# Kernel optimization log

Hardware: AMD Instinct MI355X
Metric: run time of the kernel (lower is better)

The kernel has to match this reference:

```python
import jax, jax.numpy as jnp
import numpy as np

N_PTS = 65534      # 2**16 - 2 from rand_subset
N_VARS = 24        # len(mesh.full_varlist); cols 0/1/2 = lat_deg/lon_deg/reltime_hours
RES = 1.0          # config.latent_res (degrees)
GH, GW = 180, 360  # len(latent_lats), len(latent_lons)
CL = 512           # config.latent_size
TR_DIM, TR_TOK, DEPTH, HEADS, DH = 128, 4, 2, 8, 16
PE_NUM = 8         # DEFAULT_POSEMB_NUM
DA_HALF = 12.0     # mesh.da_window_size / 2
EMB_IN = N_VARS + 3 * (1 + 2 * PE_NUM)  # 75


def setup_inputs() -> dict:
    key = jax.random.key(0)
    ks = jax.random.split(key, 12)
    feats = jax.random.normal(ks[0], (N_PTS, N_VARS), dtype=jnp.float32) * 0.5
    lat = jax.random.uniform(ks[1], (N_PTS,), minval=-90.0, maxval=90.0)
    lon = jax.random.uniform(ks[2], (N_PTS,), minval=-180.0, maxval=180.0)
    t = jax.random.uniform(ks[3], (N_PTS,), minval=-12.0, maxval=12.0)
    x = feats.at[:, 0].set(lat).at[:, 1].set(lon).at[:, 2].set(t)
    w = lambda k, s: jax.random.normal(k, s, dtype=jnp.float32) * 0.02
    return dict(
        x=x,
        W_emb=w(ks[4], (EMB_IN, TR_DIM * TR_TOK)), b_emb=jnp.zeros(TR_DIM * TR_TOK),
        ln1_s=jnp.ones((DEPTH, TR_DIM)), ln1_b=jnp.zeros((DEPTH, TR_DIM)),
        Wqkv=w(ks[5], (DEPTH, TR_DIM, 3 * TR_DIM)), bqkv=jnp.zeros((DEPTH, 3 * TR_DIM)),
        Wo=w(ks[6], (DEPTH, TR_DIM, TR_DIM)), bo=jnp.zeros((DEPTH, TR_DIM)),
        ln2_s=jnp.ones((DEPTH, TR_DIM)), ln2_b=jnp.zeros((DEPTH, TR_DIM)),
        Wf1=w(ks[7], (DEPTH, TR_DIM, 4 * TR_DIM)), bf1=jnp.zeros((DEPTH, 4 * TR_DIM)),
        Wf2=w(ks[8], (DEPTH, 4 * TR_DIM, TR_DIM)), bf2=jnp.zeros((DEPTH, TR_DIM)),
        W_comb=w(ks[9], (TR_DIM * TR_TOK, CL)), b_comb=jnp.zeros(CL),
    )


def _ln(h, s, b):
    m = jnp.mean(h, -1, keepdims=True)
    v = jnp.var(h, -1, keepdims=True)
    return (h - m) * jax.lax.rsqrt(v + 1e-5) * s + b


def _posemb(p):  # p: [N,3] -> [N, 3*(1+2*PE_NUM)]
    freqs = 2.0 ** jnp.arange(PE_NUM, dtype=p.dtype)
    ang = p[..., None] * freqs * jnp.pi  # [N,3,PE_NUM]
    n = p.shape[0]
    return jnp.concatenate([p, jnp.sin(ang).reshape(n, -1), jnp.cos(ang).reshape(n, -1)], axis=1)


def reference(x, W_emb, b_emb, ln1_s, ln1_b, Wqkv, bqkv, Wo, bo,
              ln2_s, ln2_b, Wf1, bf1, Wf2, bf2, W_comb, b_comb):
    lat = x[:, 0]
    lat = jnp.where(lat == -90.0, lat + 1e-4, lat)
    lon = x[:, 1]
    t = x[:, 2]
    # lat/lon -> latent grid indices
    lati = jnp.floor((90.0 - lat) / RES).astype(jnp.int32)
    loni = jnp.mod(180.0 / RES + jnp.floor((lon + 180.0) / RES), 360.0 / RES).astype(jnp.int32)
    # fractional cell position + relative time for sinusoidal posemb
    lat_th = jnp.mod(-lat, RES) / RES
    lon_th = jnp.mod(lon, RES) / RES
    t_th = t + 1.0
    pe = _posemb(jnp.stack([lat_th, lon_th, t_th], axis=-1))
    xn = x.at[:, 0].set(lat / 90.0).at[:, 1].set(lon / 180.0).at[:, 2].set(t / DA_HALF)
    feat = jnp.concatenate([xn, pe], axis=1)  # [N, 75]
    h = (feat @ W_emb + b_emb).reshape(-1, TR_TOK, TR_DIM)  # [N, 4, 128]
    for i in range(DEPTH):  # pre-norm transformer blocks
        a = _ln(h, ln1_s[i], ln1_b[i])
        qkv = (a @ Wqkv[i] + bqkv[i]).reshape(-1, TR_TOK, 3, HEADS, DH)
        q, k, v = qkv[:, :, 0], qkv[:, :, 1], qkv[:, :, 2]  # [N,T,H,D]
        att = jnp.einsum('nqhd,nkhd->nhqk', q, k) / np.sqrt(DH).astype(np.float32)
        att = jax.nn.softmax(att, axis=-1)
        o = jnp.einsum('nhqk,nkhd->nqhd', att, v).reshape(-1, TR_TOK, TR_DIM)
        h = h + (o @ Wo[i] + bo[i])
        f = _ln(h, ln2_s[i], ln2_b[i])
        h = h + jax.nn.gelu(f @ Wf1[i] + bf1[i]) @ Wf2[i] + bf2[i]
    y = h.reshape(-1, TR_TOK * TR_DIM) @ W_comb + b_comb  # [N, CL]
    flat = lati * GW + loni  # [N] segment ids into H*W grid
    sums = jax.ops.segment_sum(y, flat, num_segments=GH * GW)
    cnt = jax.ops.segment_sum(jnp.ones((y.shape[0],), y.dtype), flat, num_segments=GH * GW)
    reduced = sums / jnp.clip(cnt, 1.0)[:, None]  # scatter_mean semantics (empty cells -> 0)
    return reduced.reshape(1, 1, GH, GW, CL)
```

## Files before the change

### kernel.cpp

```cpp
#include <hip/hip_runtime.h>
#include <hip/hip_bf16.h>
#include <math.h>

#define N_PTS 65534
#define GH 180
#define GW 360
#define NCELL (GH*GW)
#define PI_F 3.14159265358979323846f
#define NSEC 92

typedef __bf16 bf16;
typedef bf16 bf16x8 __attribute__((ext_vector_type(8)));
typedef float f32x4 __attribute__((ext_vector_type(4)));

#define LDS_FENCE() asm volatile("s_waitcnt lgkmcnt(0)" ::: "memory")

static __device__ __forceinline__ f32x4 mfma16(bf16x8 a, bf16x8 b, f32x4 c){
    return __builtin_amdgcn_mfma_f32_16x16x32_bf16(a,b,c,0,0,0);
}

__global__ void repack_kernel(const float* __restrict__ W_emb,
                              const float* __restrict__ Wqkv,
                              const float* __restrict__ Wo,
                              const float* __restrict__ Wf1,
                              const float* __restrict__ Wf2,
                              const float* __restrict__ W_comb,
                              bf16* __restrict__ stream){
    int idx = blockIdx.x*256 + threadIdx.x;
    if (idx >= NSEC*8192) return;
    int sec = idx >> 13;
    int r   = idx & 8191;
    int u   = r >> 9;
    int e   = r & 511;
    int l   = e >> 3, j = e & 7;
    int g   = l >> 4, c = l & 15;
    float v = 0.f;
    if (sec < 8){
        if (u < 12){
            int nt=u/3, ks=u%3;
            int n = sec*64 + nt*16 + c;
            int k = ks*32 + g*8 + j;
            if (k < 75) v = W_emb[(size_t)k*512 + n];
        }
    } else if (sec < 60){
        int lay = (sec-8)/26, s = (sec-8)%26;
        if (s < 8){
            if (u < 12){
                int s3=u/4, ks=u%4;
                int col = s3*128 + s*16 + c;
                int k = ks*32 + g*8 + j;
                v = Wqkv[(size_t)lay*49152 + (size_t)k*384 + col];
            }
        } else if (s < 10){
            int nh = (s-8)*4 + u/4, ks = u%4;
            int k = ks*32 + g*8 + j;
            v = Wo[(size_t)lay*16384 + (size_t)k*128 + nh*16 + c];
        } else {
            int t = s-10, ch = t>>1;
            if (!(t&1)){
                int nt=u/4, ks=u%4;
                int n = ch*64 + nt*16 + c;
                int k = ks*32 + g*8 + j;
                v = Wf1[(size_t)lay*65536 + (size_t)k*512 + n];
            } else {
                int nt2=u/2, ks=u%2;
                int kk = ks*32 + g*8 + j;
                v = Wf2[(size_t)lay*65536 + (size_t)(ch*64+kk)*128 + nt2*16 + c];
            }
        }
    } else {
        int chk = sec-60, tk=u/4, ks=u%4;
        int n = chk*16 + c;
        int k = tk*128 + ks*32 + g*8 + j;
        v = W_comb[(size_t)k*512 + n];
    }
    stream[idx] = (bf16)v;
}

__global__ void count_kernel(const float* __restrict__ x, int* __restrict__ flat,
                             int* __restrict__ cnt){
    int p = blockIdx.x*256 + threadIdx.x;
    if (p >= N_PTS) return;
    float lat = x[p*24+0], lon = x[p*24+1];
    if (lat == -90.0f) lat += 1e-4f;
    int lati = (int)floorf(90.0f - lat);
    int loni = (180 + (int)floorf(lon + 180.0f)) % 360;
    lati = min(max(lati,0),GH-1);
    loni = min(max(loni,0),GW-1);
    int f = lati*GW + loni;
    flat[p] = f;
    atomicAdd(&cnt[f], 1);
}

#define LD12(F, sb) do{ _Pragma("unroll") for (int u=0;u<12;++u) (F)[u]=(sb)[u*64+l]; }while(0)
#define LD16(F, sb) do{ _Pragma("unroll") for (int u=0;u<16;++u) (F)[u]=(sb)[u*64+l]; }while(0)

#define P_EMB  0
#define P_QKV  512
#define P_O    1280
#define P_F1   1536
#define P_F2   2560
#define P_L1S  2816
#define P_L1B  3072
#define P_L2S  3328
#define P_L2B  3584
#define P_CMB  3840

#define EMBED_BODY(CH, F) do{ \
    const int tk_ = (CH)>>1; \
    const int hn_ = ((CH)&1)*4; \
    _Pragma("unroll") \
    for (int nt=0; nt<4; ++nt){ \
        f32x4 acc = {0.f,0.f,0.f,0.f}; \
        _Pragma("unroll") \
        for (int ks=0;ks<3;++ks) acc = mfma16(afe[ks], (F)[nt*3+ks], acc); \
        float bb = (float)prm[P_EMB + (CH)*64 + nt*16 + c]; \
        h[0][hn_+nt][tk_] = acc[0] + bb; \
        h[1][hn_+nt][tk_] = acc[1] + bb; } \
}while(0)

#define QKV_BODY(HD, F) do{ \
    f32x4 acc[3][2]; \
    _Pragma("unroll") \
    for (int s3=0;s3<3;++s3){ \
        float bias = (float)prm[P_QKV + lay*384 + s3*128 + (HD)*16 + c]; \
        _Pragma("unroll") \
        for (int mt=0;mt<2;++mt){ \
            f32x4 a = {0.f,0.f,0.f,0.f}; \
            _Pragma("unroll") \
            for (int ks=0;ks<4;++ks) a = mfma16(af[mt][ks], (F)[s3*4+ks], a); \
            _Pragma("unroll") \
            for (int j=0;j<4;++j) a[j] += bias; \
            acc[s3][mt] = a; } } \
    _Pragma("unroll") \
    for (int mt=0;mt<2;++mt){ \
        _Pragma("unroll") \
        for (int j=0;j<4;++j) acc[0][mt][j] *= 0.36067376f; \
        float att[16]; \
        _Pragma("unroll") \
        for (int i=0;i<4;++i) \
            _Pragma("unroll") \
            for (int j=0;j<4;++j){ \
                float t = acc[0][mt][i]*acc[1][mt][j]; \
                t += __shfl_xor(t,1); t += __shfl_xor(t,2); \
                t += __shfl_xor(t,4); t += __shfl_xor(t,8); \
                att[i*4+j]=t; } \
        _Pragma("unroll") \
        for (int i=0;i<4;++i){ \
            float m = fmaxf(fmaxf(att[i*4],att[i*4+1]),fmaxf(att[i*4+2],att[i*4+3])); \
            float e0=exp2f(att[i*4]-m),   e1=exp2f(att[i*4+1]-m); \
            float e2=exp2f(att[i*4+2]-m), e3=exp2f(att[i*4+3]-m); \
            float inv = __builtin_amdgcn_rcpf(e0+e1+e2+e3); \
            float o = (e0*acc[2][mt][0]+e1*acc[2][mt][1]+e2*acc[2][mt][2]+e3*acc[2][mt][3])*inv; \
            tile[wv][mt*16+g*4+i][(HD)*16+c] = (bf16)o; } } \
}while(0)

#define O_BODY(S2, F) do{ \
    _Pragma("unroll") \
    for (int n4=0;n4<4;++n4){ \
        float bias = (float)prm[P_O + lay*128 + ((S2)*4+n4)*16 + c]; \
        _Pragma("unroll") \
        for (int mt=0;mt<2;++mt){ \
            f32x4 a = h[mt][(S2)*4+n4]; \
            _Pragma("unroll") \
            for (int ks=0;ks<4;++ks) a = mfma16(oa[mt][ks], (F)[n4*4+ks], a); \
            _Pragma("unroll") \
            for (int j=0;j<4;++j) a[j]+=bias; \
            h[mt][(S2)*4+n4]=a; } } \
}while(0)

#define F1_BODY(CH, F) do{ \
    _Pragma("unroll") \
    for (int nt=0;nt<4;++nt){ \
        float bias = (float)prm[P_F1 + lay*512 + (CH)*64 + nt*16 + c]; \
        _Pragma("unroll") \
        for (int mt=0;mt<2;++mt){ \
            f32x4 a = {0.f,0.f,0.f,0.f}; \
            _Pragma("unroll") \
            for (int ks=0;ks<4;++ks) a = mfma16(f1a[mt][ks], (F)[nt*4+ks], a); \
            _Pragma("unroll") \
            for (int j=0;j<4;++j){ \
                float xx = a[j]+bias; \
                float t2 = xx*xx; \
                float pp = fmaf(t2, 0.044715f, 1.0f); \
                float w2 = xx*pp; \
                float u  = exp2f(-2.3022082f*w2); \
                float r  = __builtin_amdgcn_rcpf(1.0f+u); \
                tile[wv][mt*16+g*4+j][nt*16+c] = (bf16)(xx*r); } } } \
}while(0)

#define F2_BODY(F) do{ \
    _Pragma("unroll") \
    for (int nt2=0;nt2<8;++nt2){ \
        _Pragma("unroll") \
        for (int mt=0;mt<2;++mt){ \
            f32x4 a = h[mt][nt2]; \
            _Pragma("unroll") \
            for (int ks=0;ks<2;++ks) a = mfma16(ga[mt][ks], (F)[nt2*2+ks], a); \
            h[mt][nt2]=a; } } \
}while(0)

#define COMB_BODY(CHK, F) do{ \
    f32x4 a = {0.f,0.f,0.f,0.f}; \
    _Pragma("unroll") \
    for (int tk=0;tk<4;++tk) \
        _Pragma("unroll") \
        for (int ks=0;ks<4;++ks) a = mfma16(afc[tk][ks], (F)[tk*4+ks], a); \
    if (g<2){ \
        float bb = (float)prm[P_CMB + (CHK)*16+c]; \
        _Pragma("unroll") \
        for (int j=0;j<4;++j){ \
            int p = pb + g*4 + j; \
            if (p < N_PTS) \
                atomicAdd(&out[(size_t)flj[j]*512 + (CHK)*16 + c], (a[j]+bb)*ivj[j]); } } \
}while(0)

__global__ __launch_bounds__(256,2) void fused_kernel(
    const float* __restrict__ x,
    const bf16* __restrict__ stream,
    const float* __restrict__ b_emb, const float* __restrict__ bqkv,
    const float* __restrict__ bo,    const float* __restrict__ bf1,
    const float* __restrict__ bf2,   const float* __restrict__ b_comb,
    const float* __restrict__ ln1s,  const float* __restrict__ ln1b,
    const float* __restrict__ ln2s,  const float* __restrict__ ln2b,
    const int* __restrict__ flat,    const int* __restrict__ cnt,
    float* __restrict__ out)
{
    __shared__ __align__(16) bf16  tile[4][32][136];
    __shared__ __align__(16) bf16  prm[4352];
    const int tid = threadIdx.x;
    const int wv = tid>>6, l = tid&63;
    const int g = l>>4, c = l&15;
    const int pb = blockIdx.x*32 + wv*8;
    const bf16x8* gs8 = (const bf16x8*)stream;

    for (int i=tid; i<4352; i+=256){
        float v;
        if      (i<512)  v=b_emb[i];
        else if (i<1280) v=bqkv[i-512];
        else if (i<1536) v=bo[i-1280];
        else if (i<2560) v=bf1[i-1536];
        else if (i<2816) v=bf2[i-2560];
        else if (i<3072) v=ln1s[i-2816];
        else if (i<3328) v=ln1b[i-3072];
        else if (i<3584) v=ln2s[i-3328];
        else if (i<3840) v=ln2b[i-3584];
        else             v=b_comb[i-3840];
        prm[i]=(bf16)v;
    }

    int flj[4]; float ivj[4];
    #pragma unroll
    for (int j=0;j<4;++j){
        int p = pb + g*4 + j;
        if (g<2 && p<N_PTS){ int f=flat[p]; flj[j]=f;
            ivj[j]=__builtin_amdgcn_rcpf(fmaxf((float)cnt[f],1.f)); }
        else { flj[j]=0; ivj[j]=0.f; }
    }

    __syncthreads();

    bf16x8 wA[16], wB[16];
    LD12(wA, gs8);

    {
        const int pl = l>>3, w = l&7;
        const int p = pb + pl;
        const bool valid = (p < N_PTS);
        const int row  = (pl<4)? (pl*4)   : ((pl-4)*4+1);
        const int zrow = (pl<4)? (pl*4+2) : ((pl-4)*4+3);
        float lat=0.f, lon=0.f, t=0.f;
        if (valid){ lat=x[p*24+0]; lon=x[p*24+1]; t=x[p*24+2]; }
        if (lat == -90.0f) lat += 1e-4f;
        float pvs[3] = { -lat - floorf(-lat), lon - floorf(lon), t + 1.0f };
        #pragma unroll
        for (int i=0;i<12;++i){
            int f = w*12 + i;
            float val;
            if (f >= 75) val = 0.f;
            else if (f < 24){
                if (f==0)      val = lat*(1.f/90.f);
                else if (f==1) val = lon*(1.f/180.f);
                else if (f==2) val = t*(1.f/12.f);
                else           val = valid ? x[p*24+f] : 0.f;
            } else if (f<27) val = pvs[f-24];
            else if (f<51){ int q=f-27; val = sinf(pvs[q>>3]*(float)(1<<(q&7))*PI_F); }
            else          { int q=f-51; val = cosf(pvs[q>>3]*(float)(1<<(q&7))*PI_F); }
            if (!valid) val = 0.f;
            tile[wv][row][f]  = (bf16)val;
            tile[wv][zrow][f] = (bf16)0.f;
        }
    }
    LDS_FENCE();
    bf16x8 afe[3];
    #pragma unroll
    for (int ks=0;ks<3;++ks) afe[ks] = *(const bf16x8*)&tile[wv][c][ks*32+g*8];

    f32x4 h[2][8];
    #pragma unroll
    for (int chp=0; chp<4; ++chp){
        const int ch = chp*2;
        LD12(wB, gs8 + (size_t)(ch+1)*1024);
        EMBED_BODY(ch, wA);
        if (ch+2 < 8) LD12(wA, gs8 + (size_t)(ch+2)*1024);
        else          LD12(wA, gs8 + (size_t)8*1024);
        EMBED_BODY(ch+1, wB);
    }

    for (int lay=0; lay<2; ++lay){
        float ls[8], lb[8];
        #pragma unroll
        for (int n=0;n<8;++n){ ls[n]=(float)prm[P_L1S+lay*128+n*16+c]; lb[n]=(float)prm[P_L1B+lay*128+n*16+c]; }
        #pragma unroll
        for (int mt=0;mt<2;++mt)
            #pragma unroll
            for (int j=0;j<4;++j){
                float s=0.f,q=0.f;
                #pragma unroll
                for (int n=0;n<8;++n){ float v=h[mt][n][j]; s+=v; q+=v*v; }
                s += __shfl_xor(s,1); s += __shfl_xor(s,2); s += __shfl_xor(s,4); s += __shfl_xor(s,8);
                q += __shfl_xor(q,1); q += __shfl_xor(q,2); q += __shfl_xor(q,4); q += __shfl_xor(q,8);
                float m = s*(1.f/128.f);
                float var = q*(1.f/128.f) - m*m;
                float rs = rsqrtf(var + 1e-5f);
                #pragma unroll
                for (int n=0;n<8;++n)
                    tile[wv][mt*16+g*4+j][n*16+c] = (bf16)((h[mt][n][j]-m)*rs*ls[n]+lb[n]);
            }
        LDS_FENCE();
        bf16x8 af[2][4];
        #pragma unroll
        for (int mt=0;mt<2;++mt)
            #pragma unroll
            for (int ks=0;ks<4;++ks)
                af[mt][ks] = *(const bf16x8*)&tile[wv][mt*16+c][ks*32+g*8];
        LDS_FENCE();
        for (int hdp=0; hdp<4; ++hdp){
            const int hd = hdp*2;
            LD12(wB, gs8 + (size_t)(8 + lay*26 + hd+1)*1024);
            QKV_BODY(hd, wA);
            if (hd+2 < 8) LD12(wA, gs8 + (size_t)(8 + lay*26 + hd+2)*1024);
            else          LD16(wA, gs8 + (size_t)(8 + lay*26 + 8)*1024);
            QKV_BODY(hd+1, wB);
        }
        LDS_FENCE();
        bf16x8 oa[2][4];
        #pragma unroll
        for (int mt=0;mt<2;++mt)
            #pragma unroll
            for (int ks=0;ks<4;++ks)
                oa[mt][ks] = *(const bf16x8*)&tile[wv][mt*16+c][ks*32+g*8];
        LDS_FENCE();
        LD16(wB, gs8 + (size_t)(8 + lay*26 + 9)*1024);
        O_BODY(0, wA);
        LD16(wA, gs8 + (size_t)(8 + lay*26 + 10)*1024);
        O_BODY(1, wB);
        #pragma unroll
        for (int n=0;n<8;++n){ ls[n]=(float)prm[P_L2S+lay*128+n*16+c]; lb[n]=(float)prm[P_L2B+lay*128+n*16+c]; }
        #pragma unroll
        for (int mt=0;mt<2;++mt)
            #pragma unroll
            for (int j=0;j<4;++j){
                float s=0.f,q=0.f;
                #pragma unroll
                for (int n=0;n<8;++n){ float v=h[mt][n][j]; s+=v; q+=v*v; }
                s += __shfl_xor(s,1); s += __shfl_xor(s,2); s += __shfl_xor(s,4); s += __shfl_xor(s,8);
                q += __shfl_xor(q,1); q += __shfl_xor(q,2); q += __shfl_xor(q,4); q += __shfl_xor(q,8);
                float m = s*(1.f/128.f);
                float var = q*(1.f/128.f) - m*m;
                float rs = rsqrtf(var + 1e-5f);
                #pragma unroll
                for (int n=0;n<8;++n)
                    tile[wv][mt*16+g*4+j][n*16+c] = (bf16)((h[mt][n][j]-m)*rs*ls[n]+lb[n]);
            }
        LDS_FENCE();
        bf16x8 f1a[2][4];
        #pragma unroll
        for (int mt=0;mt<2;++mt)
            #pragma unroll
            for (int ks=0;ks<4;++ks)
                f1a[mt][ks] = *(const bf16x8*)&tile[wv][mt*16+c][ks*32+g*8];
        LDS_FENCE();
        const bf16x8* nxsec = gs8 + (size_t)((lay==0) ? (8+26) : 60)*1024;
        bf16x8 ga[2][2];
        for (int ch=0; ch<8; ++ch){
            LD16(wB, gs8 + (size_t)(8 + lay*26 + 10 + ch*2 + 1)*1024);
            F1_BODY(ch, wA);
            LDS_FENCE();
            #pragma unroll
            for (int mt=0;mt<2;++mt)
                #pragma unroll
                for (int ks=0;ks<2;++ks)
                    ga[mt][ks] = *(const bf16x8*)&tile[wv][mt*16+c][ks*32+g*8];
            LDS_FENCE();
            if (ch < 7) LD16(wA, gs8 + (size_t)(8 + lay*26 + 10 + (ch+1)*2)*1024);
            else        LD16(wA, nxsec);
            F2_BODY(wB);
        }
        #pragma unroll
        for (int nt2=0;nt2<8;++nt2){
            float bias = (float)prm[P_F2 + lay*128 + nt2*16+c];
            #pragma unroll
            for (int mt=0;mt<2;++mt)
                #pragma unroll
                for (int j=0;j<4;++j) h[mt][nt2][j]+=bias;
        }
    }

    #pragma unroll
    for (int mt=0;mt<2;++mt)
        #pragma unroll
        for (int n=0;n<8;++n)
            #pragma unroll
            for (int j=0;j<4;++j)
                tile[wv][mt*16+g*4+j][n*16+c] = (bf16)h[mt][n][j];
    LDS_FENCE();
    bf16x8 afc[4][4];
    #pragma unroll
    for (int tk=0;tk<4;++tk)
        #pragma unroll
        for (int ks=0;ks<4;++ks)
            afc[tk][ks] = *(const bf16x8*)&tile[wv][(c&7)*4+tk][ks*32+g*8];
    for (int kp=0; kp<16; ++kp){
        const int chk = kp*2;
        LD16(wB, gs8 + (size_t)(60 + chk + 1)*1024);
        COMB_BODY(chk, wA);
        if (chk+2 < 32) LD16(wA, gs8 + (size_t)(60 + chk + 2)*1024);
        COMB_BODY(chk+1, wB);
    }
}

extern "C" void kernel_launch(void* const* d_in, const int* in_sizes, int n_in,
                              void* d_out, int out_size, void* d_ws, size_t ws_size,
                              hipStream_t stream){
    (void)in_sizes; (void)n_in; (void)ws_size;
    const float* x      = (const float*)d_in[0];
    const float* W_emb  = (const float*)d_in[1];
    const float* b_emb  = (const float*)d_in[2];
    const float* ln1_s  = (const float*)d_in[3];
    const float* ln1_b  = (const float*)d_in[4];
    const float* Wqkv   = (const float*)d_in[5];
    const float* bqkv   = (const float*)d_in[6];
    const float* Wo     = (const float*)d_in[7];
    const float* bo     = (const float*)d_in[8];
    const float* ln2_s  = (const float*)d_in[9];
    const float* ln2_b  = (const float*)d_in[10];
    const float* Wf1    = (const float*)d_in[11];
    const float* bf1    = (const float*)d_in[12];
    const float* Wf2    = (const float*)d_in[13];
    const float* bf2    = (const float*)d_in[14];
    const float* W_comb = (const float*)d_in[15];
    const float* b_comb = (const float*)d_in[16];
    float* out = (float*)d_out;

    char* ws = (char*)d_ws;
    size_t off = 0;
    auto alloc = [&](size_t bytes)->char*{
        char* p = ws + off; off = (off + bytes + 255) & ~(size_t)255; return p;
    };
    bf16* wstream = (bf16*) alloc((size_t)NSEC*8192*2);
    int*  flat    = (int*)  alloc((size_t)N_PTS*4);
    int*  cnt     = (int*)  alloc((size_t)NCELL*4);

    hipMemsetAsync(d_out, 0, (size_t)out_size*sizeof(float), stream);
    hipMemsetAsync(cnt, 0, (size_t)NCELL*4, stream);

    repack_kernel<<<(NSEC*8192+255)/256, 256, 0, stream>>>(
        W_emb, Wqkv, Wo, Wf1, Wf2, W_comb, wstream);
    count_kernel<<<(N_PTS+255)/256, 256, 0, stream>>>(x, flat, cnt);

    fused_kernel<<<2048, 256, 0, stream>>>(x, wstream,
        b_emb, bqkv, bo, bf1, bf2, b_comb,
        ln1_s, ln1_b, ln2_s, ln2_b, flat, cnt, out);
}
```

Measured before the change: 808.0 us.

## Compute attention scores and weighted sum with MFMA instead of shuffle reductions

Replaces the per-head attention that used cross-lane shuffle reductions for QK^T with MFMA ops. Q and K are computed transposed so a single 16x16x32 MFMA yields block-diagonal scores, which are masked to each point's 4x4 block. A second MFMA forms P·V. The softmax scale is folded into the Wq weights and q bias at repack time. This removes many shuffle instructions but adds extra bf16 rounding of q, k, v and probabilities, plus wasted MFMA work on the zero-padded lanes.

Result: faster. 703.9 us (-12.9%).

```diff
diff --git a/kernel.cpp b/kernel.cpp
--- a/kernel.cpp
+++ b/kernel.cpp
@@ -11,6 +11,7 @@
 
 typedef __bf16 bf16;
 typedef bf16 bf16x8 __attribute__((ext_vector_type(8)));
+typedef bf16 bf16x4 __attribute__((ext_vector_type(4)));
 typedef float f32x4 __attribute__((ext_vector_type(4)));
 
 #define LDS_FENCE() asm volatile("s_waitcnt lgkmcnt(0)" ::: "memory")
@@ -50,6 +51,7 @@
                 int col = s3*128 + s*16 + c;
                 int k = ks*32 + g*8 + j;
                 v = Wqkv[(size_t)lay*49152 + (size_t)k*384 + col];
+                if (s3==0) v *= 0.36067376f;
             }
         } else if (s < 10){
             int nh = (s-8)*4 + u/4, ks = u%4;
@@ -120,39 +122,42 @@
 }while(0)
 
 #define QKV_BODY(HD, F) do{ \
-    f32x4 acc[3][2]; \
-    _Pragma("unroll") \
-    for (int s3=0;s3<3;++s3){ \
-        float bias = (float)prm[P_QKV + lay*384 + s3*128 + (HD)*16 + c]; \
-        _Pragma("unroll") \
-        for (int mt=0;mt<2;++mt){ \
-            f32x4 a = {0.f,0.f,0.f,0.f}; \
-            _Pragma("unroll") \
-            for (int ks=0;ks<4;++ks) a = mfma16(af[mt][ks], (F)[s3*4+ks], a); \
-            _Pragma("unroll") \
-            for (int j=0;j<4;++j) a[j] += bias; \
-            acc[s3][mt] = a; } } \
+    float bqv[4], bkv[4]; \
+    _Pragma("unroll") \
+    for (int r=0;r<4;++r){ \
+        bqv[r] = (float)prm[P_QKV + lay*384 +       (HD)*16 + 4*g + r]; \
+        bkv[r] = (float)prm[P_QKV + lay*384 + 128 + (HD)*16 + 4*g + r]; } \
+    float bv = (float)prm[P_QKV + lay*384 + 256 + (HD)*16 + c]; \
     _Pragma("unroll") \
     for (int mt=0;mt<2;++mt){ \
-        _Pragma("unroll") \
-        for (int j=0;j<4;++j) acc[0][mt][j] *= 0.36067376f; \
-        float att[16]; \
-        _Pragma("unroll") \
-        for (int i=0;i<4;++i) \
-            _Pragma("unroll") \
-            for (int j=0;j<4;++j){ \
-                float t = acc[0][mt][i]*acc[1][mt][j]; \
-                t += __shfl_xor(t,1); t += __shfl_xor(t,2); \
-                t += __shfl_xor(t,4); t += __shfl_xor(t,8); \
-                att[i*4+j]=t; } \
-        _Pragma("unroll") \
-        for (int i=0;i<4;++i){ \
-            float m = fmaxf(fmaxf(att[i*4],att[i*4+1]),fmaxf(att[i*4+2],att[i*4+3])); \
-            float e0=exp2f(att[i*4]-m),   e1=exp2f(att[i*4+1]-m); \
-            float e2=exp2f(att[i*4+2]-m), e3=exp2f(att[i*4+3]-m); \
-            float inv = __builtin_amdgcn_rcpf(e0+e1+e2+e3); \
-            float o = (e0*acc[2][mt][0]+e1*acc[2][mt][1]+e2*acc[2][mt][2]+e3*acc[2][mt][3])*inv; \
-            tile[wv][mt*16+g*4+i][(HD)*16+c] = (bf16)o; } } \
+        f32x4 aq={0.f,0.f,0.f,0.f}, ak={0.f,0.f,0.f,0.f}, av={0.f,0.f,0.f,0.f}; \
+        _Pragma("unroll") \
+        for (int ks=0;ks<4;++ks){ \
+            aq = mfma16((F)[ks],     af[mt][ks], aq); \
+            ak = mfma16((F)[4+ks],   af[mt][ks], ak); \
+            av = mfma16(af[mt][ks], (F)[8+ks],   av); } \
+        bf16x8 qt, kt, vt; \
+        _Pragma("unroll") \
+        for (int r=0;r<4;++r){ \
+            qt[r]=(bf16)(aq[r]+bqv[r]); qt[4+r]=(bf16)0.f; \
+            kt[r]=(bf16)(ak[r]+bkv[r]); kt[4+r]=(bf16)0.f; \
+            vt[r]=(bf16)(av[r]+bv);     vt[4+r]=(bf16)0.f; } \
+        f32x4 st = mfma16(kt, qt, (f32x4){0.f,0.f,0.f,0.f}); \
+        float m = fmaxf(fmaxf(st[0],st[1]),fmaxf(st[2],st[3])); \
+        float e0=exp2f(st[0]-m), e1=exp2f(st[1]-m); \
+        float e2=exp2f(st[2]-m), e3=exp2f(st[3]-m); \
+        float inv = __builtin_amdgcn_rcpf(e0+e1+e2+e3); \
+        float pm = pv ? inv : 0.f; \
+        bf16x8 pt; \
+        pt[0]=(bf16)(e0*pm); pt[1]=(bf16)(e1*pm); \
+        pt[2]=(bf16)(e2*pm); pt[3]=(bf16)(e3*pm); \
+        pt[4]=(bf16)0.f; pt[5]=(bf16)0.f; pt[6]=(bf16)0.f; pt[7]=(bf16)0.f; \
+        f32x4 ot = mfma16(vt, pt, (f32x4){0.f,0.f,0.f,0.f}); \
+        bf16x4 ow; \
+        _Pragma("unroll") \
+        for (int r=0;r<4;++r) ow[r]=(bf16)ot[r]; \
+        *(bf16x4*)&tile[wv][mt*16+c][(HD)*16+4*g] = ow; \
+    } \
 }while(0)
 
 #define O_BODY(S2, F) do{ \
@@ -231,13 +236,14 @@
     const int tid = threadIdx.x;
     const int wv = tid>>6, l = tid&63;
     const int g = l>>4, c = l&15;
+    const bool pv = (g == (c>>2));
     const int pb = blockIdx.x*32 + wv*8;
     const bf16x8* gs8 = (const bf16x8*)stream;
 
     for (int i=tid; i<4352; i+=256){
         float v;
         if      (i<512)  v=b_emb[i];
-        else if (i<1280) v=bqkv[i-512];
+        else if (i<1280){ v=bqkv[i-512]; if (((i-512)%384) < 128) v *= 0.36067376f; }
         else if (i<1536) v=bo[i-1280];
         else if (i<2560) v=bf1[i-1536];
         else if (i<2816) v=bf2[i-2560];
```
